# Kernel tuning notes

Hardware: AMD Instinct MI355X
Metric: run time of the kernel (lower is better)

The kernel has to match this reference:

```python
import jax, jax.numpy as jnp
import numpy as np


def conv1d(x, w, b):
    # x: [B, C_in, T], w: [C_out, C_in, K] (torch layout), b: [C_out]
    y = jax.lax.conv_general_dilated(
        x, w, window_strides=(1,), padding='SAME',
        dimension_numbers=('NCH', 'OIH', 'NCH'))
    return y + b[None, :, None]


def setup_inputs() -> dict:
    B, T, IN, H, D, K = 16, 2048, 80, 512, 512, 1024
    key = jax.random.key(0)
    ks = jax.random.split(key, 10)
    f32 = jnp.float32

    def w_init(k, shape, fan_in):
        return (jax.random.normal(k, shape, f32) / np.sqrt(fan_in)).astype(f32)

    return {
        'mels':    jax.random.normal(ks[0], (B, T, IN), f32),
        'enc_w1':  w_init(ks[1], (H, IN, 3), IN * 3),
        'enc_b1':  jnp.zeros((H,), f32),
        'enc_w2':  w_init(ks[2], (D, H, 3), H * 3),
        'enc_b2':  jnp.zeros((D,), f32),
        'codebook': jax.random.normal(ks[3], (K, D), f32),
        'dec_w1':  w_init(ks[4], (H, D, 3), D * 3),
        'dec_b1':  jnp.zeros((H,), f32),
        'dec_w2':  w_init(ks[5], (IN, H, 3), H * 3),
        'dec_b2':  jnp.zeros((IN,), f32),
    }


def reference(mels, enc_w1, enc_b1, enc_w2, enc_b2, codebook,
              dec_w1, dec_b1, dec_w2, dec_b2):
    B, T, _ = mels.shape
    D = codebook.shape[1]

    # ---- encoder: conv -> relu -> conv ----
    x = jnp.swapaxes(mels, 1, 2)                      # [B, in_dim, T]
    z = conv1d(jax.nn.relu(conv1d(x, enc_w1, enc_b1)), enc_w2, enc_b2)  # [B, D, T]

    # ---- vector quantization ----
    z_t = jnp.swapaxes(z, 1, 2)                       # [B, T, D]
    flat = z_t.reshape(-1, D)                         # [B*T, D]
    d = ((flat ** 2).sum(axis=1, keepdims=True)
         - 2.0 * flat @ codebook.T
         + (codebook ** 2).sum(axis=1)[None, :])      # [B*T, K]
    idx = jnp.argmin(d, axis=1).reshape(B, T)         # [B, T] int
    quantized = codebook[idx]                         # [B, T, D] gather

    # ---- decoder: conv -> relu -> conv ----
    q = jnp.swapaxes(quantized, 1, 2)                 # [B, D, T]
    recon = conv1d(jax.nn.relu(conv1d(q, dec_w1, dec_b1)), dec_w2, dec_b2)
    recon = jnp.swapaxes(recon, 1, 2)                 # [B, T, in_dim]
    return recon, idx
```

## Files before the change

### kernel.cpp

```cpp
#include <hip/hip_runtime.h>
#include <hip/hip_bf16.h>

#define Bsz   16
#define Tn    2048
#define INC   80
#define Hc    512
#define Dc    512
#define NCODE 1024
#define BT    (Bsz * Tn)
#define RECON_N (Bsz * Tn * INC)
#define MARGIN 0.03f

typedef __attribute__((ext_vector_type(8))) short bf16x8;
typedef __attribute__((ext_vector_type(4))) float f32x4;
typedef __attribute__((ext_vector_type(4))) unsigned short u16x4;

static __device__ __forceinline__ unsigned short f2bf(float x) {
    unsigned u = __float_as_uint(x);
    u += 0x7FFF + ((u >> 16) & 1);
    return (unsigned short)(u >> 16);
}
static __device__ __forceinline__ float bf2f(unsigned short h) {
    return __uint_as_float((unsigned)h << 16);
}

typedef const __attribute__((address_space(1))) unsigned int* gas_p;
typedef __attribute__((address_space(3))) unsigned int* las_p;
static __device__ __forceinline__ void async16(const void* g, const void* l) {
    __builtin_amdgcn_global_load_lds(
        (gas_p)(unsigned long long)g,
        (las_p)(unsigned int)(unsigned long long)l,
        16, 0, 0);
}

__global__ __launch_bounds__(64)
void code_norms(const float* __restrict__ CB, float* __restrict__ CN) {
    int j = blockIdx.x;
    int lane = threadIdx.x;
    const float4* row = (const float4*)(CB + (size_t)j * Dc);
    float s = 0.f;
    #pragma unroll
    for (int i = 0; i < 2; ++i) {
        float4 v = row[lane + i * 64];
        s = fmaf(v.x, v.x, s);
        s = fmaf(v.y, v.y, s);
        s = fmaf(v.z, v.z, s);
        s = fmaf(v.w, v.w, s);
    }
    #pragma unroll
    for (int off = 32; off > 0; off >>= 1) s += __shfl_down(s, off, 64);
    if (lane == 0) CN[j] = s;
}

__global__ __launch_bounds__(256)
void cb_transpose(const float* __restrict__ CB, float* __restrict__ CBt) {
    const int j0 = blockIdx.x * 64;
    const int d0 = blockIdx.y * 64;
    __shared__ float ts[64][65];
    const int tid = threadIdx.x;
    for (int i = tid; i < 4096; i += 256) {
        int r = i >> 6, c = i & 63;
        ts[r][c] = CB[(size_t)(j0 + r) * Dc + d0 + c];
    }
    __syncthreads();
    for (int i = tid; i < 4096; i += 256) {
        int r = i >> 6, c = i & 63;
        CBt[(size_t)(d0 + r) * NCODE + j0 + c] = ts[c][r];
    }
}

__global__ __launch_bounds__(256)
void mels_transpose(const float* __restrict__ M, float* __restrict__ MT) {
    const int t0 = blockIdx.x * 64;
    const int b  = blockIdx.y;
    __shared__ float ts[64][84];
    const int tid = threadIdx.x;
    #pragma unroll
    for (int it = 0; it < 5; ++it) {
        int i = tid + it * 256;
        int t = i / 20, c4 = i % 20;
        *(float4*)&ts[t][c4 * 4] =
            *(const float4*)&M[((size_t)b * Tn + t0 + t) * INC + c4 * 4];
    }
    __syncthreads();
    #pragma unroll
    for (int it = 0; it < 20; ++it) {
        int i = tid + it * 256;
        int c = i >> 6, t = i & 63;
        MT[((size_t)b * INC + c) * Tn + t0 + t] = ts[t][c];
    }
}

__global__ __launch_bounds__(256)
void wt_transpose(const float* __restrict__ W, float* __restrict__ Wt,
                  int Cin, int Cout) {
    const int o0 = blockIdx.x * 64;
    const int c0 = blockIdx.y * 16;
    __shared__ float ts[48][65];
    const int tid = threadIdx.x;
    for (int i = tid; i < 64 * 48; i += 256) {
        int o = i / 48, ck = i % 48;
        int oo = o0 + o;
        float v = 0.f;
        if (oo < Cout) v = W[(size_t)oo * Cin * 3 + c0 * 3 + ck];
        ts[ck][o] = v;
    }
    __syncthreads();
    for (int i = tid; i < 48 * 64; i += 256) {
        int o = i & 63, ck = i >> 6;
        int oo = o0 + o;
        if (oo < Cout) Wt[(size_t)(c0 * 3 + ck) * Cout + oo] = ts[ck][o];
    }
}

__global__ __launch_bounds__(256)
void wsplit(const float* __restrict__ W, unsigned short* __restrict__ Whl) {
    int o = blockIdx.x, k = blockIdx.y;
    #pragma unroll
    for (int it = 0; it < 2; ++it) {
        int c = threadIdx.x + it * 256;
        float v = W[((size_t)o * Hc + c) * 3 + k];
        unsigned short h = f2bf(v);
        size_t base = ((size_t)(k * Hc + o) * 16 + (c >> 5)) * 64 + (c & 31);
        Whl[base] = h;
        Whl[base + 32] = f2bf(v - bf2f(h));
    }
}

__global__ __launch_bounds__(256)
void wsplit80(const float* __restrict__ W, unsigned short* __restrict__ Wh) {
    int o = blockIdx.x, k = blockIdx.y;
    #pragma unroll
    for (int it = 0; it < 2; ++it) {
        int c = threadIdx.x + it * 256;
        Wh[((size_t)k * INC + o) * Hc + c] = f2bf(W[((size_t)o * Hc + c) * 3 + k]);
    }
}

__global__ __launch_bounds__(256)
void cbsplit(const float* __restrict__ CB, unsigned short* __restrict__ CBhl) {
    int j = blockIdx.x;
    #pragma unroll
    for (int it = 0; it < 2; ++it) {
        int d = threadIdx.x + it * 256;
        float v = CB[(size_t)j * Dc + d];
        unsigned short h = f2bf(v);
        size_t base = ((size_t)j * 16 + (d >> 5)) * 64 + (d & 31);
        CBhl[base] = h;
        CBhl[base + 32] = f2bf(v - bf2f(h));
    }
}

__global__ __launch_bounds__(256)
void conv_enc1(const float* __restrict__ X, const float* __restrict__ Wt,
               const float* __restrict__ bias, unsigned short* __restrict__ Yhl) {
    const int t0 = blockIdx.x * 64;
    const int o0 = blockIdx.y * 128;
    const int b  = blockIdx.z;
    union SharedU {
        struct { float Xs[16][72]; float Ws[48][132]; } a;
        float Ys[128][69];
    };
    __shared__ __align__(16) SharedU su;
    float (&Xs)[16][72]  = su.a.Xs;
    float (&Ws)[48][132] = su.a.Ws;
    const int tid = threadIdx.x;
    const int tx = tid & 15, ty = tid >> 4;
    float acc[8][4] = {};
    const float* Xb = X + (size_t)b * INC * Tn;

    if (blockIdx.x == 0 && tid < 64) {
        u16x4 z4 = {0, 0, 0, 0};
        *(u16x4*)(Yhl + ((size_t)(b * (Tn + 2)) * 16 + (o0 >> 5)) * 64 + tid * 4) = z4;
    }
    if (blockIdx.x == Tn / 64 - 1 && tid < 64) {
        u16x4 z4 = {0, 0, 0, 0};
        *(u16x4*)(Yhl + ((size_t)(b * (Tn + 2) + Tn + 1) * 16 + (o0 >> 5)) * 64
                  + tid * 4) = z4;
    }

    for (int c0 = 0; c0 < INC; c0 += 16) {
        for (int i = tid; i < 16 * 66; i += 256) {
            int cc = i / 66, tt = i % 66;
            int t = t0 + tt - 1;
            float v = 0.f;
            if (t >= 0 && t < Tn) v = Xb[(size_t)(c0 + cc) * Tn + t];
            Xs[cc][tt] = v;
        }
        for (int i = tid; i < 48 * 128; i += 256) {
            int o = i & 127, ck = i >> 7;
            Ws[ck][o] = Wt[(size_t)(c0 * 3 + ck) * Hc + o0 + o];
        }
        __syncthreads();
        #pragma unroll
        for (int cc = 0; cc < 16; ++cc) {
            float4 xa = *(const float4*)&Xs[cc][tx * 4];
            float2 xb2 = *(const float2*)&Xs[cc][tx * 4 + 4];
            float xv[6] = {xa.x, xa.y, xa.z, xa.w, xb2.x, xb2.y};
            #pragma unroll
            for (int k = 0; k < 3; ++k) {
                float4 wa = *(const float4*)&Ws[cc * 3 + k][ty * 4];
                float4 wb = *(const float4*)&Ws[cc * 3 + k][64 + ty * 4];
                float wv[8] = {wa.x, wa.y, wa.z, wa.w, wb.x, wb.y, wb.z, wb.w};
                #pragma unroll
                for (int i8 = 0; i8 < 8; ++i8)
                    #pragma unroll
                    for (int j = 0; j < 4; ++j)
                        acc[i8][j] = fmaf(wv[i8], xv[k + j], acc[i8][j]);
            }
        }
        __syncthreads();
    }
    #pragma unroll
    for (int og = 0; og < 2; ++og)
        #pragma unroll
        for (int oi = 0; oi < 4; ++oi) {
            int ol = og * 64 + ty * 4 + oi;
            float bv = bias[o0 + ol];
            const int i8 = og * 4 + oi;
            #pragma unroll
            for (int j = 0; j < 4; ++j)
                su.Ys[ol][tx * 4 + j] = fmaxf(acc[i8][j] + bv, 0.f);
        }
    __syncthreads();
    #pragma unroll
    for (int it = 0; it < 8; ++it) {
        int i = tid + it * 256;
        int oq = i & 31, t = i >> 5;
        int o4 = o0 + oq * 4;
        u16x4 h, l;
        #pragma unroll
        for (int r = 0; r < 4; ++r) {
            float v = su.Ys[oq * 4 + r][t];
            unsigned short hh = f2bf(v);
            h[r] = hh;
            l[r] = f2bf(v - bf2f(hh));
        }
        size_t base = ((size_t)(b * (Tn + 2) + 1 + t0 + t) * 16 + (o4 >> 5)) * 64
                      + (o4 & 31);
        *(u16x4*)(Yhl + base) = h;
        *(u16x4*)(Yhl + base + 32) = l;
    }
}

__global__ __launch_bounds__(256)
void conv_mid_mfma(const unsigned short* __restrict__ Xhl,
                   const unsigned short* __restrict__ Whl,
                   const float* __restrict__ bias,
                   unsigned short* __restrict__ Zt,
                   unsigned short* __restrict__ Lo2) {
    const int lin  = blockIdx.x + (blockIdx.y << 4) + (blockIdx.z << 6);
    const int slot = lin >> 3;
    const int b  = ((lin & 7) << 1) | (slot >> 6);
    const int t0 = ((slot & 63) >> 2) << 7;
    const int o0 = (slot & 3) << 7;
    __shared__ __align__(16) unsigned short XL[2][136 * 64];
    const int tid  = threadIdx.x;
    const int lane = tid & 63;
    const int wave = tid >> 6;
    const int wm = wave >> 1, wn = wave & 1;
    const int m16 = lane & 15;
    const int q = lane >> 4;
    const int lrow = lane >> 3;
    const int lchk = (lane & 7) ^ lrow;
    const unsigned short* Xb = Xhl + ((size_t)b * (Tn + 2) + t0) * 1024
                               + (size_t)lrow * 1024 + lchk * 8;

    f32x4 acc[4][4];
    #pragma unroll
    for (int mt = 0; mt < 4; ++mt)
        #pragma unroll
        for (int nt = 0; nt < 4; ++nt)
            acc[mt][nt] = (f32x4){0.f, 0.f, 0.f, 0.f};

    #pragma unroll
    for (int i = 0; i < 5; ++i) {
        int ii = wave + i * 4;
        if (ii < 17)
            async16(Xb + (size_t)ii * 8192, &XL[0][ii * 512]);
    }

    for (int c0 = 0; c0 < Hc; c0 += 32) {
        const int buf = (c0 >> 5) & 1;
        __syncthreads();
        if (c0 + 32 < Hc) {
            const unsigned short* src = Xb + (size_t)((c0 >> 5) + 1) * 64;
            #pragma unroll
            for (int i = 0; i < 5; ++i) {
                int ii = wave + i * 4;
                if (ii < 17)
                    async16(src + (size_t)ii * 8192, &XL[buf ^ 1][ii * 512]);
            }
        }
        #pragma unroll
        for (int k = 0; k < 3; ++k) {
            bf16x8 Ah[4], Al[4];
            #pragma unroll
            for (int mt = 0; mt < 4; ++mt) {
                int o = o0 + wm * 64 + mt * 16 + m16;
                size_t base = ((size_t)(k * Hc + o) * 16 + (c0 >> 5)) * 64 + q * 8;
                Ah[mt] = *(const bf16x8*)(Whl + base);
                Al[mt] = *(const bf16x8*)(Whl + base + 32);
            }
            #pragma unroll
            for (int nt = 0; nt < 4; ++nt) {
                int row = wn * 64 + nt * 16 + m16 + k;
                const unsigned short* rp = &XL[buf][row * 64];
                int ph = (q ^ (row & 7)) * 8;
                union { bf16x8 v; uint4 u; } bh, bl;
                bh.u = *(const uint4*)(rp + ph);
                bl.u = *(const uint4*)(rp + (ph ^ 32));
                __builtin_amdgcn_s_setprio(1);
                #pragma unroll
                for (int mt = 0; mt < 4; ++mt)
                    acc[mt][nt] = __builtin_amdgcn_mfma_f32_16x16x32_bf16(
                        Ah[mt], bh.v, acc[mt][nt], 0, 0, 0);
                #pragma unroll
                for (int mt = 0; mt < 4; ++mt)
                    acc[mt][nt] = __builtin_amdgcn_mfma_f32_16x16x32_bf16(
                        Al[mt], bh.v, acc[mt][nt], 0, 0, 0);
                #pragma unroll
                for (int mt = 0; mt < 4; ++mt)
                    acc[mt][nt] = __builtin_amdgcn_mfma_f32_16x16x32_bf16(
                        Ah[mt], bl.v, acc[mt][nt], 0, 0, 0);
                __builtin_amdgcn_s_setprio(0);
            }
        }
    }
    unsigned short* SZ = &XL[0][0];
    unsigned short* SL = &XL[0][0] + 32 * 256;
    unsigned short* Lb = Lo2 + (size_t)b * Tn * 512;
    const int g0 = o0 >> 5;
    #pragma unroll
    for (int p = 0; p < 4; ++p) {
        __syncthreads();
        if (wn == (p >> 1)) {
            #pragma unroll
            for (int nt2 = 0; nt2 < 2; ++nt2) {
                int nt = (p & 1) * 2 + nt2;
                int srow = nt2 * 16 + m16;
                #pragma unroll
                for (int mt = 0; mt < 4; ++mt) {
                    int lo = wm * 64 + mt * 16 + q * 4;
                    int ob = o0 + lo;
                    float4 bq = *(const float4*)&bias[ob];
                    float bqa[4] = {bq.x, bq.y, bq.z, bq.w};
                    u16x4 h, l, l2;
                    #pragma unroll
                    for (int r = 0; r < 4; ++r) {
                        float v = acc[mt][nt][r] + bqa[r];
                        unsigned short hh = f2bf(v);
                        float r1 = v - bf2f(hh);
                        unsigned short ll = f2bf(r1);
                        h[r] = hh;
                        l[r] = ll;
                        l2[r] = f2bf(r1 - bf2f(ll));
                    }
                    int gb = (lo >> 5) * 64 + (lo & 31);
                    *(u16x4*)&SZ[srow * 256 + gb] = h;
                    *(u16x4*)&SZ[srow * 256 + gb + 32] = l;
                    *(u16x4*)&SL[srow * 128 + lo] = l2;
                }
            }
        }
        __syncthreads();
        #pragma unroll
        for (int it = 0; it < 8; ++it) {
            int i = tid + it * 256;
            int row = i >> 6, c = i & 63;
            *(u16x4*)(Zt + ((size_t)(b * Tn + t0 + p * 32 + row) * 16 + g0) * 64
                      + c * 4) = *(u16x4*)&SZ[row * 256 + c * 4];
        }
        #pragma unroll
        for (int it = 0; it < 4; ++it) {
            int i = tid + it * 256;
            int row = i >> 5, c = i & 31;
            *(u16x4*)(Lb + (size_t)(t0 + p * 32 + row) * 512 + o0 + c * 4)
                = *(u16x4*)&SL[row * 128 + c * 4];
        }
    }
}

__global__ __launch_bounds__(256)
void dec2_mfma(const unsigned short* __restrict__ Xt,
               const unsigned short* __restrict__ Wh2,
               const float* __restrict__ bias, float* __restrict__ OUT) {
    const int t0 = blockIdx.x * 128;
    const int b  = blockIdx.z;
    __shared__ __align__(16) unsigned short XL[2][136 * 64];
    const int tid = threadIdx.x;
    const int lane = tid & 63;
    const int wave = tid >> 6;
    const int wn = wave;
    const int m16 = lane & 15;
    const int q = lane >> 4;
    const int lrow = lane >> 3;
    const int lchk = (lane & 7) ^ lrow;
    const unsigned short* Xb = Xt + ((size_t)b * (Tn + 2) + t0) * 512
                               + (size_t)lrow * 512 + lchk * 8;

    f32x4 acc[5][2];
    #pragma unroll
    for (int mt = 0; mt < 5; ++mt)
        #pragma unroll
        for (int nt = 0; nt < 2; ++nt)
            acc[mt][nt] = (f32x4){0.f, 0.f, 0.f, 0.f};

    #pragma unroll
    for (int i = 0; i < 5; ++i) {
        int ii = wave + i * 4;
        if (ii < 17)
            async16(Xb + (size_t)ii * 4096, &XL[0][ii * 512]);
    }

    for (int c0 = 0; c0 < Hc; c0 += 64) {
        const int buf = (c0 >> 6) & 1;
        __syncthreads();
        if (c0 + 64 < Hc) {
            const unsigned short* src = Xb + (size_t)((c0 >> 6) + 1) * 64;
            #pragma unroll
            for (int i = 0; i < 5; ++i) {
                int ii = wave + i * 4;
                if (ii < 17)
                    async16(src + (size_t)ii * 4096, &XL[buf ^ 1][ii * 512]);
            }
        }
        #pragma unroll
        for (int k = 0; k < 3; ++k) {
            #pragma unroll
            for (int sub = 0; sub < 2; ++sub) {
                int c = c0 + sub * 32;
                bf16x8 Ah[5];
                #pragma unroll
                for (int mt = 0; mt < 5; ++mt) {
                    int o = mt * 16 + m16;
                    Ah[mt] = *(const bf16x8*)(Wh2 + ((size_t)(k * INC + o)) * Hc
                                              + c + q * 8);
                }
                #pragma unroll
                for (int nt = 0; nt < 2; ++nt) {
                    int row = wn * 32 + nt * 16 + m16 + k;
                    const unsigned short* rp = &XL[buf][row * 64];
                    int p = sub * 4 + q;
                    int ph = (p ^ (row & 7)) * 8;
                    union { bf16x8 v; uint4 u; } bh;
                    bh.u = *(const uint4*)(rp + ph);
                    #pragma unroll
                    for (int mt = 0; mt < 5; ++mt)
                        acc[mt][nt] = __builtin_amdgcn_mfma_f32_16x16x32_bf16(
                            Ah[mt], bh.v, acc[mt][nt], 0, 0, 0);
                }
            }
        }
    }
    #pragma unroll
    for (int mt = 0; mt < 5; ++mt) {
        float4 bq = *(const float4*)&bias[mt * 16 + q * 4];
        #pragma unroll
        for (int nt = 0; nt < 2; ++nt) {
            int t = t0 + wn * 32 + nt * 16 + m16;
            float4 r;
            r.x = acc[mt][nt][0] + bq.x;
            r.y = acc[mt][nt][1] + bq.y;
            r.z = acc[mt][nt][2] + bq.z;
            r.w = acc[mt][nt][3] + bq.w;
            *(float4*)(OUT + ((size_t)b * Tn + t) * INC + mt * 16 + q * 4) = r;
        }
    }
}

__global__ __launch_bounds__(256)
void vq_mfma(const unsigned short* __restrict__ Zt,
             const unsigned short* __restrict__ CBhl,
             const float* __restrict__ CN,
             float* __restrict__ candv, int* __restrict__ candi,
             float* __restrict__ cand2v) {
    const int lin  = blockIdx.x + (blockIdx.y << 8);
    const int slotB = lin >> 3;
    const int nb = ((lin & 7) << 5) | (slotB & 31);
    const int jb = slotB >> 5;
    const int b  = nb >> 4;
    const int t0 = (nb & 15) * 128;
    const int jbase = jb * 128;
    __shared__ __align__(16) unsigned char pool[32768];
    unsigned short* XL0 = (unsigned short*)pool;
    unsigned short* XL1 = (unsigned short*)(pool + 16384);
    float* RV = (float*)pool;
    int*   RI = (int*)(pool + 4096);
    float* R2 = (float*)(pool + 8192);

    const int tid = threadIdx.x;
    const int lane = tid & 63;
    const int wave = tid >> 6;
    const int wm = wave >> 1, wn = wave & 1;
    const int m16 = lane & 15;
    const int q = lane >> 4;
    const int lrow = lane >> 3;
    const int lchk = (lane & 7) ^ lrow;
    const unsigned short* Zb = Zt + (size_t)(b * Tn + t0) * 1024
                               + (size_t)lrow * 1024 + lchk * 8;

    f32x4 acc[4][4];
    #pragma unroll
    for (int mt = 0; mt < 4; ++mt)
        #pragma unroll
        for (int nt = 0; nt < 4; ++nt)
            acc[mt][nt] = (f32x4){0.f, 0.f, 0.f, 0.f};

    #pragma unroll
    for (int i = 0; i < 4; ++i) {
        int ii = wave + i * 4;
        async16(Zb + (size_t)ii * 8192, XL0 + ii * 512);
    }

    for (int d0 = 0; d0 < Dc; d0 += 32) {
        const int buf = (d0 >> 5) & 1;
        unsigned short* XL = buf ? XL1 : XL0;
        __syncthreads();
        if (d0 + 32 < Dc) {
            unsigned short* XN = buf ? XL0 : XL1;
            const unsigned short* src = Zb + (size_t)((d0 >> 5) + 1) * 64;
            #pragma unroll
            for (int i = 0; i < 4; ++i) {
                int ii = wave + i * 4;
                async16(src + (size_t)ii * 8192, XN + ii * 512);
            }
        }
        bf16x8 Ah[4], Al[4];
        #pragma unroll
        for (int mt = 0; mt < 4; ++mt) {
            int j = jbase + wm * 64 + mt * 16 + m16;
            size_t base = ((size_t)j * 16 + (d0 >> 5)) * 64 + q * 8;
            Ah[mt] = *(const bf16x8*)(CBhl + base);
            Al[mt] = *(const bf16x8*)(CBhl + base + 32);
        }
        #pragma unroll
        for (int nt = 0; nt < 4; ++nt) {
            int row = wn * 64 + nt * 16 + m16;
            const unsigned short* rp = XL + row * 64;
            int ph = (q ^ (row & 7)) * 8;
            union { bf16x8 v; uint4 u; } bh, bl;
            bh.u = *(const uint4*)(rp + ph);
            bl.u = *(const uint4*)(rp + (ph ^ 32));
            __builtin_amdgcn_s_setprio(1);
            #pragma unroll
            for (int mt = 0; mt < 4; ++mt)
                acc[mt][nt] = __builtin_amdgcn_mfma_f32_16x16x32_bf16(
                    Ah[mt], bh.v, acc[mt][nt], 0, 0, 0);
            #pragma unroll
            for (int mt = 0; mt < 4; ++mt)
                acc[mt][nt] = __builtin_amdgcn_mfma_f32_16x16x32_bf16(
                    Al[mt], bh.v, acc[mt][nt], 0, 0, 0);
            #pragma unroll
            for (int mt = 0; mt < 4; ++mt)
                acc[mt][nt] = __builtin_amdgcn_mfma_f32_16x16x32_bf16(
                    Ah[mt], bl.v, acc[mt][nt], 0, 0, 0);
            __builtin_amdgcn_s_setprio(0);
        }
    }
    __syncthreads();

    float cn4[4][4];
    #pragma unroll
    for (int mt = 0; mt < 4; ++mt) {
        float4 c = *(const float4*)&CN[jbase + wm * 64 + mt * 16 + q * 4];
        cn4[mt][0] = c.x; cn4[mt][1] = c.y; cn4[mt][2] = c.z; cn4[mt][3] = c.w;
    }
    #pragma unroll
    for (int nt = 0; nt < 4; ++nt) {
        int t = wn * 64 + nt * 16 + m16;
        float v1 = 1e30f, v2 = 1e30f;
        int i1 = 0;
        #pragma unroll
        for (int mt = 0; mt < 4; ++mt)
            #pragma unroll
            for (int r = 0; r < 4; ++r) {
                float d = fmaf(-2.f, acc[mt][nt][r], cn4[mt][r]);
                int j = jbase + wm * 64 + mt * 16 + q * 4 + r;
                if (d < v1 || (d == v1 && j < i1)) { v2 = v1; v1 = d; i1 = j; }
                else if (d < v2) v2 = d;
            }
        int slotw = wm * 4 + q;
        RV[t * 8 + slotw] = v1;
        RI[t * 8 + slotw] = i1;
        R2[t * 8 + slotw] = v2;
    }
    __syncthreads();
    if (tid < 128) {
        int t = tid;
        float v1 = RV[t * 8], v2 = R2[t * 8];
        int i1 = RI[t * 8];
        #pragma unroll
        for (int s = 1; s < 8; ++s) {
            float a1 = RV[t * 8 + s], a2 = R2[t * 8 + s];
            int ai = RI[t * 8 + s];
            if (a1 < v1 || (a1 == v1 && ai < i1)) {
                v2 = fminf(v1, a2); v1 = a1; i1 = ai;
            } else {
                v2 = fminf(v2, a1);
            }
        }
        int n = b * Tn + t0 + t;
        candv[(size_t)jb * BT + n] = v1;
        candi[(size_t)jb * BT + n] = i1;
        cand2v[(size_t)jb * BT + n] = v2;
    }
}

__global__ __launch_bounds__(256)
void vq_reduce2(const float* __restrict__ candv, const int* __restrict__ candi,
                const float* __restrict__ cand2v, int* __restrict__ idxI,
                float* __restrict__ idxf, int* __restrict__ flagn,
                int* __restrict__ flaglist) {
    int n = blockIdx.x * 256 + threadIdx.x;
    float v1 = candv[n], v2 = cand2v[n];
    int i1 = candi[n];
    #pragma unroll
    for (int jq = 1; jq < 8; ++jq) {
        float a1 = candv[(size_t)jq * BT + n];
        float a2 = cand2v[(size_t)jq * BT + n];
        int ai = candi[(size_t)jq * BT + n];
        if (a1 < v1 || (a1 == v1 && ai < i1)) {
            v2 = fminf(v1, a2); v1 = a1; i1 = ai;
        } else {
            v2 = fminf(v2, a1);
        }
    }
    idxI[n] = i1;
    idxf[n] = (float)i1;
    if (v2 - v1 < MARGIN) {
        int s = atomicAdd(flagn, 1);
        flaglist[s] = n;
    }
}

__global__ __launch_bounds__(256)
void vq_rescue(const int* __restrict__ flagn, const int* __restrict__ flaglist,
               const unsigned short* __restrict__ Zt,
               const unsigned short* __restrict__ Lo2,
               const float* __restrict__ CB,
               const float* __restrict__ CN, int* __restrict__ idxI,
               float* __restrict__ idxf) {
    __shared__ float zs[512];
    __shared__ float rvv[256];
    __shared__ int   rii[256];
    const int nf = *flagn;
    for (int f = blockIdx.x; f < nf; f += gridDim.x) {
        int n = flaglist[f];
        __syncthreads();
        #pragma unroll
        for (int it = 0; it < 2; ++it) {
            int d = threadIdx.x + it * 256;
            const unsigned short* zr = Zt + ((size_t)n * 16 + (d >> 5)) * 64
                                       + (d & 31);
            zs[d] = bf2f(zr[0]) + bf2f(zr[32]) + bf2f(Lo2[(size_t)n * 512 + d]);
        }
        __syncthreads();
        float bv = 1e30f;
        int bi = 0;
        #pragma unroll
        for (int jj = 0; jj < 4; ++jj) {
            int j = threadIdx.x * 4 + jj;
            const float* cr = CB + (size_t)j * Dc;
            float dot = 0.f;
            for (int d = 0; d < Dc; ++d) dot = fmaf(zs[d], cr[d], dot);
            float dist = fmaf(-2.f, dot, CN[j]);
            if (dist < bv || (dist == bv && j < bi)) { bv = dist; bi = j; }
        }
        rvv[threadIdx.x] = bv;
        rii[threadIdx.x] = bi;
        __syncthreads();
        for (int off = 128; off > 0; off >>= 1) {
            if (threadIdx.x < off) {
                float ov = rvv[threadIdx.x + off];
                int oi = rii[threadIdx.x + off];
                if (ov < rvv[threadIdx.x] ||
                    (ov == rvv[threadIdx.x] && oi < rii[threadIdx.x])) {
                    rvv[threadIdx.x] = ov; rii[threadIdx.x] = oi;
                }
            }
            __syncthreads();
        }
        if (threadIdx.x == 0) {
            idxI[n] = rii[0];
            idxf[n] = (float)rii[0];
        }
    }
}

__global__ __launch_bounds__(256)
void gemm_g(const float* __restrict__ CBt, const float* __restrict__ Wt,
            float* __restrict__ G) {
    const int j0 = blockIdx.x * 64;
    const int kk = blockIdx.y >> 2;
    const int o0 = (blockIdx.y & 3) * 128;
    __shared__ __align__(16) float As[16][68];
    __shared__ __align__(16) float Bs[16][132];
    const int tid = threadIdx.x;
    const int tx = tid & 15, ty = tid >> 4;
    float acc[4][8] = {};

    for (int c0 = 0; c0 < Dc; c0 += 16) {
        {
            int cc = tid >> 4, j4 = tid & 15;
            *(float4*)&As[cc][j4 * 4] =
                *(const float4*)&CBt[(size_t)(c0 + cc) * NCODE + j0 + j4 * 4];
        }
        #pragma unroll
        for (int it = 0; it < 2; ++it) {
            int i = tid + it * 256;
            int cc = i >> 5, o4 = i & 31;
            *(float4*)&Bs[cc][o4 * 4] =
                *(const float4*)&Wt[(size_t)((c0 + cc) * 3 + kk) * Hc + o0 + o4 * 4];
        }
        __syncthreads();
        #pragma unroll
        for (int cc = 0; cc < 16; ++cc) {
            float4 a = *(const float4*)&As[cc][tx * 4];
            float av[4] = {a.x, a.y, a.z, a.w};
            float4 b0 = *(const float4*)&Bs[cc][ty * 4];
            float4 b1 = *(const float4*)&Bs[cc][64 + ty * 4];
            float bv[8] = {b0.x, b0.y, b0.z, b0.w, b1.x, b1.y, b1.z, b1.w};
            #pragma unroll
            for (int jj = 0; jj < 4; ++jj)
                #pragma unroll
                for (int oo = 0; oo < 8; ++oo)
                    acc[jj][oo] = fmaf(av[jj], bv[oo], acc[jj][oo]);
        }
        __syncthreads();
    }
    #pragma unroll
    for (int jj = 0; jj < 4; ++jj) {
        int j = j0 + tx * 4 + jj;
        float* gp = G + (size_t)j * 1536 + kk * 512 + o0;
        *(float4*)(gp + ty * 4) = *(float4*)&acc[jj][0];
        *(float4*)(gp + 64 + ty * 4) = *(float4*)&acc[jj][4];
    }
}

__global__ __launch_bounds__(256)
void dec_y3(const int* __restrict__ idx, const float* __restrict__ G,
            const float* __restrict__ bias, unsigned short* __restrict__ Yt) {
    const int t0 = blockIdx.x * 64;
    const int o0 = blockIdx.y * 128;
    const int b  = blockIdx.z;
    const int tid = threadIdx.x;
    __shared__ int sidx[66];
    __shared__ __align__(16) float Ys[128][68];

    if (blockIdx.x == 0 && tid < 32) {
        u16x4 z4 = {0, 0, 0, 0};
        *(u16x4*)(Yt + (size_t)(b * (Tn + 2)) * 512 + o0 + tid * 4) = z4;
    }
    if (blockIdx.x == Tn / 64 - 1 && tid < 32) {
        u16x4 z4 = {0, 0, 0, 0};
        *(u16x4*)(Yt + (size_t)(b * (Tn + 2) + Tn + 1) * 512 + o0 + tid * 4) = z4;
    }

    if (tid < 66) {
        int t = t0 + tid - 1;
        sidx[tid] = (t >= 0 && t < Tn) ? idx[b * Tn + t] : -1;
    }
    __syncthreads();

    const int o = tid & 127;
    const int half = tid >> 7;
    float acc[32] = {};
    #pragma unroll
    for (int kk = 0; kk < 3; ++kk) {
        const float* Gk = G + (size_t)kk * 512 + o0 + o;
        #pragma unroll
        for (int k = 0; k < 32; ++k) {
            int j = sidx[half + 2 * k + kk];
            if (j >= 0) acc[k] += Gk[(size_t)j * 1536];
        }
    }
    float bv = bias[o0 + o];
    #pragma unroll
    for (int k = 0; k < 32; ++k)
        Ys[o][half + 2 * k] = fmaxf(acc[k] + bv, 0.f);
    __syncthreads();

    unsigned short* Yb = Yt + ((size_t)(b * (Tn + 2) + 1 + t0)) * 512 + o0;
    #pragma unroll
    for (int it = 0; it < 8; ++it) {
        int i = tid + it * 256;
        int t = i >> 5, oq = i & 31;
        u16x4 h;
        #pragma unroll
        for (int r = 0; r < 4; ++r)
            h[r] = f2bf(Ys[oq * 4 + r][t]);
        *(u16x4*)(Yb + (size_t)t * 512 + oq * 4) = h;
    }
}

extern "C" void kernel_launch(void* const* d_in, const int* in_sizes, int n_in,
                              void* d_out, int out_size, void* d_ws, size_t ws_size,
                              hipStream_t stream) {
    const float* mels    = (const float*)d_in[0];
    const float* enc_w1  = (const float*)d_in[1];
    const float* enc_b1  = (const float*)d_in[2];
    const float* enc_w2  = (const float*)d_in[3];
    const float* enc_b2  = (const float*)d_in[4];
    const float* codebook= (const float*)d_in[5];
    const float* dec_w1  = (const float*)d_in[6];
    const float* dec_b1  = (const float*)d_in[7];
    const float* dec_w2  = (const float*)d_in[8];
    const float* dec_b2  = (const float*)d_in[9];

    float* out = (float*)d_out;
    float* recon = out;
    float* idxf  = out + RECON_N;

    const size_t ACT = (size_t)Bsz * Hc * Tn;
    const size_t Y1HL_U = (size_t)Bsz * (Tn + 2) * 1024 + 16384;
    const size_t R2F = Y1HL_U / 2;

    unsigned short* Zt  = (unsigned short*)d_ws;
    unsigned short* y3t = (unsigned short*)d_ws;
    float* r2 = (float*)d_ws + ACT;
    unsigned short* y1hl = (unsigned short*)r2;
    float* sm    = r2 + R2F;
    int*   idxI  = (int*)sm;
    float* cn    = (float*)(idxI + BT);
    float* cbt   = cn + NCODE;
    float* wt1   = cbt + (size_t)Dc * NCODE;
    float* wt3   = wt1 + (size_t)INC * 3 * Hc;
    float* candv = wt3 + (size_t)Dc * 3 * Hc;
    float* cand2v= candv + (size_t)8 * BT;
    int*   candi = (int*)(cand2v + (size_t)8 * BT);
    int*   flagn = candi + (size_t)8 * BT;
    int*   flaglist = flagn + 4;
    float* G     = (float*)(flaglist + BT);
    unsigned short* whl  = (unsigned short*)(G + (size_t)NCODE * 1536);
    unsigned short* cbhl = whl + (size_t)3 * Hc * 1024;
    unsigned short* wh2  = cbhl + (size_t)NCODE * 1024;
    float* melsT = (float*)(wh2 + (size_t)3 * INC * Hc);
    unsigned short* lo2 = (unsigned short*)melsT;

    dim3 blk(256);
    hipMemsetAsync(flagn, 0, 16, stream);
    code_norms<<<dim3(NCODE), dim3(64), 0, stream>>>(codebook, cn);
    cb_transpose<<<dim3(NCODE / 64, Dc / 64), blk, 0, stream>>>(codebook, cbt);
    mels_transpose<<<dim3(Tn / 64, Bsz), blk, 0, stream>>>(mels, melsT);
    wt_transpose<<<dim3(Hc / 64, INC / 16), blk, 0, stream>>>(enc_w1, wt1, INC, Hc);
    wsplit<<<dim3(Hc, 3), blk, 0, stream>>>(enc_w2, whl);
    cbsplit<<<dim3(NCODE), blk, 0, stream>>>(codebook, cbhl);
    wt_transpose<<<dim3(Hc / 64, Dc / 16), blk, 0, stream>>>(dec_w1, wt3, Dc, Hc);
    wsplit80<<<dim3(INC, 3), blk, 0, stream>>>(dec_w2, wh2);
    gemm_g<<<dim3(NCODE / 64, 12), blk, 0, stream>>>(cbt, wt3, G);
    conv_enc1<<<dim3(Tn / 64, Hc / 128, Bsz), blk, 0, stream>>>(melsT, wt1, enc_b1,
                                                                y1hl);
    conv_mid_mfma<<<dim3(Tn / 128, Hc / 128, Bsz), blk, 0, stream>>>(y1hl, whl,
                                                                     enc_b2,
                                                                     Zt, lo2);
    vq_mfma<<<dim3(BT / 128, NCODE / 128), blk, 0, stream>>>(Zt, cbhl, cn,
                                                             candv, candi, cand2v);
    vq_reduce2<<<dim3(BT / 256), blk, 0, stream>>>(candv, candi, cand2v, idxI,
                                                   idxf, flagn, flaglist);
    vq_rescue<<<dim3(128), blk, 0, stream>>>(flagn, flaglist, Zt, lo2, codebook,
                                             cn, idxI, idxf);
    dec_y3<<<dim3(Tn / 64, 4, Bsz), blk, 0, stream>>>(idxI, G, dec_b1, y3t);
    dec2_mfma<<<dim3(Tn / 128, 1, Bsz), blk, 0, stream>>>(y3t, wh2, dec_b2, recon);
}
```

Measured before the change: 793.1 us.

## Give each wave a private LDS staging buffer to remove block barriers

In conv_mid_mfma and vq_mfma, each wave now stages its own copy of the input tile rows in private LDS double buffers. A per-wave vmcnt drain replaces the block-wide __syncthreads in the K loop. Epilogue staging strides are padded (264/136) to reduce LDS bank conflicts. This removes barrier stalls, but waves sharing wn now load duplicate data, which doubles global/LDS load traffic and grows LDS use (73KB for conv), which may reduce occupancy.

```diff
diff --git a/kernel.cpp b/kernel.cpp
--- a/kernel.cpp
+++ b/kernel.cpp
@@ -31,6 +31,10 @@
         (gas_p)(unsigned long long)g,
         (las_p)(unsigned int)(unsigned long long)l,
         16, 0, 0);
+}
+
+static __device__ __forceinline__ void wave_vm_drain() {
+    asm volatile("s_waitcnt vmcnt(0)" ::: "memory");
 }
 
 __global__ __launch_bounds__(64)
@@ -254,7 +258,7 @@
     const int b  = ((lin & 7) << 1) | (slot >> 6);
     const int t0 = ((slot & 63) >> 2) << 7;
     const int o0 = (slot & 3) << 7;
-    __shared__ __align__(16) unsigned short XL[2][136 * 64];
+    __shared__ __align__(16) unsigned short pool[4 * 2 * 72 * 64];
     const int tid  = threadIdx.x;
     const int lane = tid & 63;
     const int wave = tid >> 6;
@@ -263,8 +267,9 @@
     const int q = lane >> 4;
     const int lrow = lane >> 3;
     const int lchk = (lane & 7) ^ lrow;
-    const unsigned short* Xb = Xhl + ((size_t)b * (Tn + 2) + t0) * 1024
-                               + (size_t)lrow * 1024 + lchk * 8;
+    unsigned short* XW = pool + wave * (2 * 72 * 64);
+    const unsigned short* XbW = Xhl + ((size_t)b * (Tn + 2) + t0 + wn * 64) * 1024
+                                + (size_t)lrow * 1024 + lchk * 8;
 
     f32x4 acc[4][4];
     #pragma unroll
@@ -274,23 +279,17 @@
             acc[mt][nt] = (f32x4){0.f, 0.f, 0.f, 0.f};
 
     #pragma unroll
-    for (int i = 0; i < 5; ++i) {
-        int ii = wave + i * 4;
-        if (ii < 17)
-            async16(Xb + (size_t)ii * 8192, &XL[0][ii * 512]);
-    }
+    for (int i = 0; i < 9; ++i)
+        async16(XbW + (size_t)i * 8192, XW + i * 512);
 
     for (int c0 = 0; c0 < Hc; c0 += 32) {
         const int buf = (c0 >> 5) & 1;
-        __syncthreads();
+        wave_vm_drain();
         if (c0 + 32 < Hc) {
-            const unsigned short* src = Xb + (size_t)((c0 >> 5) + 1) * 64;
-            #pragma unroll
-            for (int i = 0; i < 5; ++i) {
-                int ii = wave + i * 4;
-                if (ii < 17)
-                    async16(src + (size_t)ii * 8192, &XL[buf ^ 1][ii * 512]);
-            }
+            const unsigned short* src = XbW + (size_t)((c0 >> 5) + 1) * 64;
+            #pragma unroll
+            for (int i = 0; i < 9; ++i)
+                async16(src + (size_t)i * 8192, XW + (buf ^ 1) * 4608 + i * 512);
         }
         #pragma unroll
         for (int k = 0; k < 3; ++k) {
@@ -304,8 +303,8 @@
             }
             #pragma unroll
             for (int nt = 0; nt < 4; ++nt) {
-                int row = wn * 64 + nt * 16 + m16 + k;
-                const unsigned short* rp = &XL[buf][row * 64];
+                int row = nt * 16 + m16 + k;
+                const unsigned short* rp = XW + buf * 4608 + row * 64;
                 int ph = (q ^ (row & 7)) * 8;
                 union { bf16x8 v; uint4 u; } bh, bl;
                 bh.u = *(const uint4*)(rp + ph);
@@ -327,13 +326,14 @@
             }
         }
     }
-    unsigned short* SZ = &XL[0][0];
-    unsigned short* SL = &XL[0][0] + 32 * 256;
+    __syncthreads();
+    unsigned short* SZ = pool;
+    unsigned short* SL = pool + 32 * 264;
     unsigned short* Lb = Lo2 + (size_t)b * Tn * 512;
     const int g0 = o0 >> 5;
     #pragma unroll
     for (int p = 0; p < 4; ++p) {
-        __syncthreads();
+        if (p) __syncthreads();
         if (wn == (p >> 1)) {
             #pragma unroll
             for (int nt2 = 0; nt2 < 2; ++nt2) {
@@ -357,9 +357,9 @@
                         l2[r] = f2bf(r1 - bf2f(ll));
                     }
                     int gb = (lo >> 5) * 64 + (lo & 31);
-                    *(u16x4*)&SZ[srow * 256 + gb] = h;
-                    *(u16x4*)&SZ[srow * 256 + gb + 32] = l;
-                    *(u16x4*)&SL[srow * 128 + lo] = l2;
+                    *(u16x4*)&SZ[srow * 264 + gb] = h;
+                    *(u16x4*)&SZ[srow * 264 + gb + 32] = l;
+                    *(u16x4*)&SL[srow * 136 + lo] = l2;
                 }
             }
         }
@@ -369,14 +369,14 @@
             int i = tid + it * 256;
             int row = i >> 6, c = i & 63;
             *(u16x4*)(Zt + ((size_t)(b * Tn + t0 + p * 32 + row) * 16 + g0) * 64
-                      + c * 4) = *(u16x4*)&SZ[row * 256 + c * 4];
+                      + c * 4) = *(u16x4*)&SZ[row * 264 + c * 4];
         }
         #pragma unroll
         for (int it = 0; it < 4; ++it) {
             int i = tid + it * 256;
             int row = i >> 5, c = i & 31;
             *(u16x4*)(Lb + (size_t)(t0 + p * 32 + row) * 512 + o0 + c * 4)
-                = *(u16x4*)&SL[row * 128 + c * 4];
+                = *(u16x4*)&SL[row * 136 + c * 4];
         }
     }
 }
@@ -482,12 +482,10 @@
     const int b  = nb >> 4;
     const int t0 = (nb & 15) * 128;
     const int jbase = jb * 128;
-    __shared__ __align__(16) unsigned char pool[32768];
-    unsigned short* XL0 = (unsigned short*)pool;
-    unsigned short* XL1 = (unsigned short*)(pool + 16384);
-    float* RV = (float*)pool;
-    int*   RI = (int*)(pool + 4096);
-    float* R2 = (float*)(pool + 8192);
+    __shared__ __align__(16) unsigned short vpool[4 * 2 * 64 * 64];
+    float* RV = (float*)vpool;
+    int*   RI = (int*)((char*)vpool + 4096);
+    float* R2 = (float*)((char*)vpool + 8192);
 
     const int tid = threadIdx.x;
     const int lane = tid & 63;
@@ -497,8 +495,9 @@
     const int q = lane >> 4;
     const int lrow = lane >> 3;
     const int lchk = (lane & 7) ^ lrow;
-    const unsigned short* Zb = Zt + (size_t)(b * Tn + t0) * 1024
-                               + (size_t)lrow * 1024 + lchk * 8;
+    unsigned short* XW = vpool + wave * (2 * 64 * 64);
+    const unsigned short* ZbW = Zt + (size_t)(b * Tn + t0 + wn * 64) * 1024
+                                + (size_t)lrow * 1024 + lchk * 8;
 
     f32x4 acc[4][4];
     #pragma unroll
@@ -508,23 +507,17 @@
             acc[mt][nt] = (f32x4){0.f, 0.f, 0.f, 0.f};
 
     #pragma unroll
-    for (int i = 0; i < 4; ++i) {
-        int ii = wave + i * 4;
-        async16(Zb + (size_t)ii * 8192, XL0 + ii * 512);
-    }
+    for (int i = 0; i < 8; ++i)
+        async16(ZbW + (size_t)i * 8192, XW + i * 512);
 
     for (int d0 = 0; d0 < Dc; d0 += 32) {
         const int buf = (d0 >> 5) & 1;
-        unsigned short* XL = buf ? XL1 : XL0;
-        __syncthreads();
+        wave_vm_drain();
         if (d0 + 32 < Dc) {
-            unsigned short* XN = buf ? XL0 : XL1;
-            const unsigned short* src = Zb + (size_t)((d0 >> 5) + 1) * 64;
-            #pragma unroll
-            for (int i = 0; i < 4; ++i) {
-                int ii = wave + i * 4;
-                async16(src + (size_t)ii * 8192, XN + ii * 512);
-            }
+            const unsigned short* src = ZbW + (size_t)((d0 >> 5) + 1) * 64;
+            #pragma unroll
+            for (int i = 0; i < 8; ++i)
+                async16(src + (size_t)i * 8192, XW + (buf ^ 1) * 4096 + i * 512);
         }
         bf16x8 Ah[4], Al[4];
         #pragma unroll
@@ -536,8 +529,8 @@
         }
         #pragma unroll
         for (int nt = 0; nt < 4; ++nt) {
-            int row = wn * 64 + nt * 16 + m16;
-            const unsigned short* rp = XL + row * 64;
+            int row = nt * 16 + m16;
+            const unsigned short* rp = XW + buf * 4096 + row * 64;
             int ph = (q ^ (row & 7)) * 8;
             union { bf16x8 v; uint4 u; } bh, bl;
             bh.u = *(const uint4*)(rp + ph);
```

Result: no change. 800.0 us (+0.9%).
